# Optimization experiments

Hardware: AMD Instinct MI355X
Metric: run time of the kernel (lower is better)

Reference implementation:

```python
import jax, jax.numpy as jnp
import numpy as np

N, DIM, E = 2048, 16, 65536


def setup_inputs() -> dict:
    key = jax.random.key(0)
    k1, k2, k3, k4 = jax.random.split(key, 4)
    emb_nodes = jax.random.normal(k1, (N, DIM), dtype=jnp.float32)
    edge_list = jax.random.randint(k2, (2, E), 0, N, dtype=jnp.int32)
    # nn.Linear(2*dim, 1): weight [1, 2*dim], bias [1]
    bound = 1.0 / np.sqrt(2 * DIM)
    W = jax.random.uniform(k3, (1, 2 * DIM), minval=-bound, maxval=bound, dtype=jnp.float32)
    b = jax.random.uniform(k4, (1,), minval=-bound, maxval=bound, dtype=jnp.float32)
    return {"emb_nodes": emb_nodes, "edge_list": edge_list, "W": W, "b": b}


def reference(emb_nodes, edge_list, W, b):
    n, d = emb_nodes.shape
    # torch code detaches the pairwise embeddings -> stop_gradient here
    e = jax.lax.stop_gradient(emb_nodes)
    # pair p = i*n + j : first node i, second node j
    interleaved = jnp.repeat(e, n, axis=0)          # [n*n, d] = e[i]
    repeated = jnp.tile(e, (n, 1))                  # [n*n, d] = e[j]
    edge_embeddings = jnp.concatenate([interleaved, repeated], axis=1)  # [n*n, 2d]
    # self-loop mask: |e[i]-e[j]| sums to 0 (i.e. identical embeddings)
    non_empty_mask = jnp.abs(interleaved - repeated).sum(axis=1) > 0    # [n*n] bool
    edge_logits = edge_embeddings @ W.T + b         # [n*n, 1]
    logits_without_self_loops = jnp.where(non_empty_mask, edge_logits[:, 0], -10.0)
    # vectorized membership: pair (i,j) is a true edge iff it appears in edge_list
    # (embeddings drawn from a continuous dist are distinct a.s., so equality of
    # concatenated embeddings <=> equality of (i,j) index pairs)
    flat_idx = edge_list[0].astype(jnp.int32) * n + edge_list[1].astype(jnp.int32)
    true_edges = jnp.zeros((n * n,), dtype=jnp.float32).at[flat_idx].set(1.0)
    return edge_embeddings, logits_without_self_loops, true_edges
```

## Files before the change

### kernel.cpp

```cpp
#include <hip/hip_runtime.h>

constexpr int NN = 2048;
constexpr int NE = 65536;

constexpr int THREADS       = 256;
constexpr int BLOCKS        = 4096;
constexpr int TOTAL_THREADS = THREADS * BLOCKS;
constexpr int TOTAL_Q       = NN * NN * 8;
constexpr int ITERS_A       = TOTAL_Q / TOTAL_THREADS;
constexpr int TOTAL4        = NN * NN / 4;

typedef float f32x4 __attribute__((ext_vector_type(4)));

__global__ __launch_bounds__(256) void fused_streams_kernel(
    const f32x4* __restrict__ emb4,
    const float* __restrict__ W,
    const float* __restrict__ bptr,
    f32x4* __restrict__ out_emb4,
    f32x4* __restrict__ logits4,
    f32x4* __restrict__ true4) {
    const int tid = blockIdx.x * blockDim.x + threadIdx.x;

    for (int o = 0; o < ITERS_A / 8; ++o) {
        const int qb = tid + o * 8 * TOTAL_THREADS;
        f32x4 v[8];
#pragma unroll
        for (int u = 0; u < 8; ++u) {
            const int q  = qb + u * TOTAL_THREADS;
            const int p  = q >> 3;
            const int c4 = q & 7;
            const int i  = p >> 11;
            const int j  = p & (NN - 1);
            const int row = (c4 < 4) ? i : j;
            v[u] = emb4[row * 4 + (c4 & 3)];
        }
#pragma unroll
        for (int u = 0; u < 8; ++u) {
            const int q = qb + u * TOTAL_THREADS;
            __builtin_nontemporal_store(v[u], &out_emb4[q]);
        }
    }

    {
        const int t  = tid;
        const int p0 = t << 2;
        const int i  = p0 >> 11;
        const int j0 = p0 & (NN - 1);

        const f32x4* w  = reinterpret_cast<const f32x4*>(W);
        const f32x4* ri = emb4 + i * 4;
        float a = 0.f;
#pragma unroll
        for (int k = 0; k < 4; ++k) {
            f32x4 r = ri[k], wl = w[k];
            a += r.x * wl.x + r.y * wl.y + r.z * wl.z + r.w * wl.w;
        }
        float cvals[4];
#pragma unroll
        for (int jj = 0; jj < 4; ++jj) {
            const f32x4* rj = emb4 + (j0 + jj) * 4;
            float s = 0.f;
#pragma unroll
            for (int k = 0; k < 4; ++k) {
                f32x4 r = rj[k], wh = w[k + 4];
                s += r.x * wh.x + r.y * wh.y + r.z * wh.z + r.w * wh.w;
            }
            cvals[jj] = s;
        }
        const float base = a + bptr[0];
        f32x4 o;
        o.x = (j0 + 0 == i) ? -10.0f : base + cvals[0];
        o.y = (j0 + 1 == i) ? -10.0f : base + cvals[1];
        o.z = (j0 + 2 == i) ? -10.0f : base + cvals[2];
        o.w = (j0 + 3 == i) ? -10.0f : base + cvals[3];
        __builtin_nontemporal_store(o, &logits4[t]);
        f32x4 z = {0.f, 0.f, 0.f, 0.f};
        true4[t] = z;
    }
}

__global__ __launch_bounds__(256) void scatter_kernel(
    const int* __restrict__ el, float* __restrict__ true_e) {
    int t = blockIdx.x * blockDim.x + threadIdx.x;
    if (t >= NE) return;
    int i = el[t];
    int j = el[NE + t];
    true_e[i * NN + j] = 1.0f;
}

extern "C" void kernel_launch(void* const* d_in, const int* in_sizes, int n_in,
                              void* d_out, int out_size, void* d_ws, size_t ws_size,
                              hipStream_t stream) {
    const float* emb = (const float*)d_in[0];
    const int*   el  = (const int*)d_in[1];
    const float* W   = (const float*)d_in[2];
    const float* b   = (const float*)d_in[3];

    float* out        = (float*)d_out;
    float* out_emb    = out;
    float* out_logits = out + (size_t)NN * NN * 32;
    float* out_true   = out_logits + (size_t)NN * NN;

    fused_streams_kernel<<<BLOCKS, THREADS, 0, stream>>>(
        (const f32x4*)emb, W, b,
        (f32x4*)out_emb, (f32x4*)out_logits, (f32x4*)out_true);

    scatter_kernel<<<(NE + THREADS - 1) / THREADS, THREADS, 0, stream>>>(el, out_true);
}
```

Measured before the change: 594.6 us.

## Split fused stream kernel into separate embedding and logits kernels

Splits the single fused kernel into an embedding-pair copy kernel, run on twice as many blocks with a fully unrolled loop, and a separate logits/zero-fill kernel. Nontemporal stores are replaced with regular stores. The aim is a simpler, better-balanced streaming write of the large embedding output, at the cost of an extra kernel launch and possibly more cache pollution from the regular stores.

```diff
diff --git a/kernel.cpp b/kernel.cpp
--- a/kernel.cpp
+++ b/kernel.cpp
@@ -3,30 +3,24 @@
 constexpr int NN = 2048;
 constexpr int NE = 65536;
 
-constexpr int THREADS       = 256;
-constexpr int BLOCKS        = 4096;
-constexpr int TOTAL_THREADS = THREADS * BLOCKS;
-constexpr int TOTAL_Q       = NN * NN * 8;
-constexpr int ITERS_A       = TOTAL_Q / TOTAL_THREADS;
-constexpr int TOTAL4        = NN * NN / 4;
-
 typedef float f32x4 __attribute__((ext_vector_type(4)));
 
-__global__ __launch_bounds__(256) void fused_streams_kernel(
-    const f32x4* __restrict__ emb4,
-    const float* __restrict__ W,
-    const float* __restrict__ bptr,
-    f32x4* __restrict__ out_emb4,
-    f32x4* __restrict__ logits4,
-    f32x4* __restrict__ true4) {
+constexpr int EMB_BLOCKS  = 8192;
+constexpr int EMB_THREADS = 256;
+constexpr int EMB_TOTAL_T = EMB_BLOCKS * EMB_THREADS;
+constexpr int TOTAL_Q     = NN * NN * 8;
+constexpr int EMB_GROUPS  = TOTAL_Q / (EMB_TOTAL_T * 8);
+
+__global__ __launch_bounds__(256) void emb_pairs_kernel(
+    const f32x4* __restrict__ emb4, f32x4* __restrict__ out4) {
     const int tid = blockIdx.x * blockDim.x + threadIdx.x;
-
-    for (int o = 0; o < ITERS_A / 8; ++o) {
-        const int qb = tid + o * 8 * TOTAL_THREADS;
+#pragma unroll
+    for (int o = 0; o < EMB_GROUPS; ++o) {
+        const int qb = tid + o * 8 * EMB_TOTAL_T;
         f32x4 v[8];
 #pragma unroll
         for (int u = 0; u < 8; ++u) {
-            const int q  = qb + u * TOTAL_THREADS;
+            const int q  = qb + u * EMB_TOTAL_T;
             const int p  = q >> 3;
             const int c4 = q & 7;
             const int i  = p >> 11;
@@ -36,47 +30,49 @@
         }
 #pragma unroll
         for (int u = 0; u < 8; ++u) {
-            const int q = qb + u * TOTAL_THREADS;
-            __builtin_nontemporal_store(v[u], &out_emb4[q]);
+            out4[qb + u * EMB_TOTAL_T] = v[u];
         }
     }
+}
 
-    {
-        const int t  = tid;
-        const int p0 = t << 2;
-        const int i  = p0 >> 11;
-        const int j0 = p0 & (NN - 1);
+__global__ __launch_bounds__(256) void logits_kernel(
+    const f32x4* __restrict__ emb4, const float* __restrict__ W,
+    const float* __restrict__ bptr, f32x4* __restrict__ logits4,
+    f32x4* __restrict__ true4) {
+    const int t  = blockIdx.x * blockDim.x + threadIdx.x;
+    const int p0 = t << 2;
+    const int i  = p0 >> 11;
+    const int j0 = p0 & (NN - 1);
 
-        const f32x4* w  = reinterpret_cast<const f32x4*>(W);
-        const f32x4* ri = emb4 + i * 4;
-        float a = 0.f;
+    const f32x4* w  = reinterpret_cast<const f32x4*>(W);
+    const f32x4* ri = emb4 + i * 4;
+    float a = 0.f;
+#pragma unroll
+    for (int k = 0; k < 4; ++k) {
+        f32x4 r = ri[k], wl = w[k];
+        a += r.x * wl.x + r.y * wl.y + r.z * wl.z + r.w * wl.w;
+    }
+    float cvals[4];
+#pragma unroll
+    for (int jj = 0; jj < 4; ++jj) {
+        const f32x4* rj = emb4 + (j0 + jj) * 4;
+        float s = 0.f;
 #pragma unroll
         for (int k = 0; k < 4; ++k) {
-            f32x4 r = ri[k], wl = w[k];
-            a += r.x * wl.x + r.y * wl.y + r.z * wl.z + r.w * wl.w;
+            f32x4 r = rj[k], wh = w[k + 4];
+            s += r.x * wh.x + r.y * wh.y + r.z * wh.z + r.w * wh.w;
         }
-        float cvals[4];
-#pragma unroll
-        for (int jj = 0; jj < 4; ++jj) {
-            const f32x4* rj = emb4 + (j0 + jj) * 4;
-            float s = 0.f;
-#pragma unroll
-            for (int k = 0; k < 4; ++k) {
-                f32x4 r = rj[k], wh = w[k + 4];
-                s += r.x * wh.x + r.y * wh.y + r.z * wh.z + r.w * wh.w;
-            }
-            cvals[jj] = s;
-        }
-        const float base = a + bptr[0];
-        f32x4 o;
-        o.x = (j0 + 0 == i) ? -10.0f : base + cvals[0];
-        o.y = (j0 + 1 == i) ? -10.0f : base + cvals[1];
-        o.z = (j0 + 2 == i) ? -10.0f : base + cvals[2];
-        o.w = (j0 + 3 == i) ? -10.0f : base + cvals[3];
-        __builtin_nontemporal_store(o, &logits4[t]);
-        f32x4 z = {0.f, 0.f, 0.f, 0.f};
-        true4[t] = z;
+        cvals[jj] = s;
     }
+    const float base = a + bptr[0];
+    f32x4 o;
+    o.x = (j0 + 0 == i) ? -10.0f : base + cvals[0];
+    o.y = (j0 + 1 == i) ? -10.0f : base + cvals[1];
+    o.z = (j0 + 2 == i) ? -10.0f : base + cvals[2];
+    o.w = (j0 + 3 == i) ? -10.0f : base + cvals[3];
+    logits4[t] = o;
+    f32x4 z = {0.f, 0.f, 0.f, 0.f};
+    true4[t] = z;
 }
 
 __global__ __launch_bounds__(256) void scatter_kernel(
@@ -101,9 +97,11 @@
     float* out_logits = out + (size_t)NN * NN * 32;
     float* out_true   = out_logits + (size_t)NN * NN;
 
-    fused_streams_kernel<<<BLOCKS, THREADS, 0, stream>>>(
-        (const f32x4*)emb, W, b,
-        (f32x4*)out_emb, (f32x4*)out_logits, (f32x4*)out_true);
+    emb_pairs_kernel<<<EMB_BLOCKS, EMB_THREADS, 0, stream>>>(
+        (const f32x4*)emb, (f32x4*)out_emb);
 
-    scatter_kernel<<<(NE + THREADS - 1) / THREADS, THREADS, 0, stream>>>(el, out_true);
+    logits_kernel<<<NN * NN / 4 / 256, 256, 0, stream>>>(
+        (const f32x4*)emb, W, b, (f32x4*)out_logits, (f32x4*)out_true);
+
+    scatter_kernel<<<NE / 256, 256, 0, stream>>>(el, out_true);
 }
```

New measurement: 602.2 us. Within noise of the previous version (+1.3%).
